# Kernel tuning notes

Measured on AMD Instinct MI355X. Metric: run time of the kernel, lower is better.

Reference implementation:

```python
import jax, jax.numpy as jnp
import numpy as np

B, P, D, H = 4, 2048, 768, 12  # batch, patches, patch_dims, heads
HD = D // H
EPS = 1e-5


def _layernorm(x, g, b):
    mu = jnp.mean(x, axis=-1, keepdims=True)
    var = jnp.mean(jnp.square(x - mu), axis=-1, keepdims=True)
    return (x - mu) * jax.lax.rsqrt(var + EPS) * g + b


def setup_inputs() -> dict:
    key = jax.random.key(0)
    ks = jax.random.split(key, 4)
    s = 0.02
    return {
        "x": jax.random.normal(ks[0], (B, P, D), jnp.float32),
        "ln1_w": jnp.ones((D,), jnp.float32),
        "ln1_b": jnp.zeros((D,), jnp.float32),
        "w_qkv": jax.random.normal(ks[1], (D, 3 * D), jnp.float32) * s,
        "b_qkv": jnp.zeros((3 * D,), jnp.float32),
        "ln2_w": jnp.ones((D,), jnp.float32),
        "ln2_b": jnp.zeros((D,), jnp.float32),
        "w_fc1": jax.random.normal(ks[2], (D, 4 * D), jnp.float32) * s,
        "b_fc1": jnp.zeros((4 * D,), jnp.float32),
        "w_fc2": jax.random.normal(ks[3], (4 * D, D), jnp.float32) * s,
        "b_fc2": jnp.zeros((D,), jnp.float32),
    }


def reference(x, ln1_w, ln1_b, w_qkv, b_qkv, ln2_w, ln2_b, w_fc1, b_fc1, w_fc2, b_fc2):
    scale = HD ** -0.5
    # --- attention block (pre-norm) ---
    residual = x
    h = _layernorm(x, ln1_w, ln1_b)
    qkv = h @ w_qkv + b_qkv                              # (B, P, 3D)
    qkv = qkv.reshape(B, P, 3, H, HD).transpose(2, 0, 3, 1, 4)  # (3, B, H, P, HD)
    q, k, v = qkv[0], qkv[1], qkv[2]
    attn = jnp.einsum('bhpd,bhqd->bhpq', q, k) * scale   # (B, H, P, P)
    # NOTE: original uses nn.Softmax(dim=1) -> normalizes over HEADS axis
    attn = jax.nn.softmax(attn, axis=1)
    out = jnp.einsum('bhpq,bhqd->bhpd', attn, v)         # (B, H, P, HD)
    out = out.transpose(0, 2, 1, 3).reshape(B, P, D)
    x = out + residual
    # --- MLP block (pre-norm) ---
    residual = x
    h = _layernorm(x, ln2_w, ln2_b)
    h = jax.nn.gelu(h @ w_fc1 + b_fc1, approximate=False)
    h = h @ w_fc2 + b_fc2
    return h + residual
```

## Files before the change

### kernel.cpp

```cpp
#include <hip/hip_runtime.h>
#include <hip/hip_bf16.h>

typedef __bf16 bf8 __attribute__((ext_vector_type(8)));
typedef float f4 __attribute__((ext_vector_type(4)));
typedef unsigned short u16;
typedef unsigned int u32;

#define B_ 4
#define P_ 2048
#define D_ 768
#define H_ 12
#define HD_ 64
#define EXPC_ 0.18033688011112042f

typedef const __attribute__((address_space(1))) void gvoid;
typedef __attribute__((address_space(3))) void lvoid;

__device__ __forceinline__ void gl_lds16(const u16* g, u16* l) {
  __builtin_amdgcn_global_load_lds((gvoid*)g, (lvoid*)l, 16, 0, 0);
}

__device__ __forceinline__ u16 f2bf(float f) {
  union { float f; u32 u; } c; c.f = f;
  u32 u = c.u;
  u += 0x7fffu + ((u >> 16) & 1u);
  return (u16)(u >> 16);
}

__device__ __forceinline__ float bf2f(u16 v) {
  union { u32 u; float f; } c; c.u = (u32)v << 16; return c.f;
}

__device__ __forceinline__ uint2 pack4(f4 v) {
  union { float f; u32 u; } a, b, c, d;
  a.f = v[0]; b.f = v[1]; c.f = v[2]; d.f = v[3];
  uint2 r;
  r.x = (a.u >> 16) | (b.u & 0xffff0000u);
  r.y = (c.u >> 16) | (d.u & 0xffff0000u);
  return r;
}

__device__ __forceinline__ f4 unpack4(ushort4 v) {
  f4 r;
  r[0] = bf2f(v.x); r[1] = bf2f(v.y); r[2] = bf2f(v.z); r[3] = bf2f(v.w);
  return r;
}

__device__ __forceinline__ f4 unp2(uint2 u) {
  f4 r;
  r[0] = bf2f((u16)(u.x & 0xffffu)); r[1] = bf2f((u16)(u.x >> 16));
  r[2] = bf2f((u16)(u.y & 0xffffu)); r[3] = bf2f((u16)(u.y >> 16));
  return r;
}

__device__ __forceinline__ bf8 mkbf8(f4 a, f4 b) {
  union { uint4 u; bf8 v; } c;
  uint2 l = pack4(a), h = pack4(b);
  c.u = make_uint4(l.x, l.y, h.x, h.y);
  return c.v;
}

__device__ __forceinline__ f4 mfma16(bf8 a, bf8 b, f4 c) {
  return __builtin_amdgcn_mfma_f32_16x16x32_bf16(a, b, c, 0, 0, 0);
}

#define ZERO44(acc)                    \
  {                                    \
    f4 z_ = {0.f, 0.f, 0.f, 0.f};      \
    for (int i_ = 0; i_ < 4; ++i_)     \
      for (int j_ = 0; j_ < 4; ++j_)   \
        acc[i_][j_] = z_;              \
  }

__device__ __forceinline__ int xcd_swz(int lin, int nwg) {
  return (lin & 7) * (nwg >> 3) + (lin >> 3);
}

__global__ __launch_bounds__(256) void prep_k(const float* __restrict__ wqkv, u16* __restrict__ wqkvT,
                                              const float* __restrict__ wfc1, u16* __restrict__ wfc1T,
                                              const float* __restrict__ wfc2, u16* __restrict__ wfc2T,
                                              const float* __restrict__ x, const float* __restrict__ g,
                                              const float* __restrict__ b, u16* __restrict__ hln) {
  __shared__ float t[32][33];
  __shared__ float a[4], a2[4];
  int id = blockIdx.x;
  if (id >= 6336) {
    int row = id - 6336;
    const float* xr = x + (size_t)row * D_;
    float v0 = xr[threadIdx.x], v1 = xr[threadIdx.x + 256], v2 = xr[threadIdx.x + 512];
    float s = v0 + v1 + v2;
    float s2 = v0 * v0 + v1 * v1 + v2 * v2;
    #pragma unroll
    for (int o = 32; o > 0; o >>= 1) {
      s += __shfl_down(s, o, 64);
      s2 += __shfl_down(s2, o, 64);
    }
    int wv = threadIdx.x >> 6;
    if ((threadIdx.x & 63) == 0) { a[wv] = s; a2[wv] = s2; }
    __syncthreads();
    s = a[0] + a[1] + a[2] + a[3];
    s2 = a2[0] + a2[1] + a2[2] + a2[3];
    float mean = s * (1.f / 768.f);
    float var = s2 * (1.f / 768.f) - mean * mean;
    float rstd = rsqrtf(var + 1e-5f);
    u16* orow = hln + (size_t)row * D_;
    float vv[3] = {v0, v1, v2};
    #pragma unroll
    for (int j = 0; j < 3; ++j) {
      int i = threadIdx.x + j * 256;
      orow[i] = f2bf((vv[j] - mean) * rstd * g[i] + b[i]);
    }
    return;
  }
  const float* src;
  u16* dst;
  int R, C, bx, by;
  if (id < 1728) {
    src = wqkv; dst = wqkvT; R = 768; C = 2304; bx = id % 72; by = id / 72;
  } else if (id < 4032) {
    int j = id - 1728;
    src = wfc1; dst = wfc1T; R = 768; C = 3072; bx = j % 96; by = j / 96;
  } else {
    int j = id - 4032;
    src = wfc2; dst = wfc2T; R = 3072; C = 768; bx = j % 24; by = j / 24;
  }
  int c0 = bx * 32, r0 = by * 32;
  int tx = threadIdx.x & 31, ty = threadIdx.x >> 5;
  #pragma unroll
  for (int i = 0; i < 32; i += 8) {
    int r = r0 + ty + i, c = c0 + tx;
    t[ty + i][tx] = (r < R && c < C) ? src[(size_t)r * C + c] : 0.f;
  }
  __syncthreads();
  #pragma unroll
  for (int i = 0; i < 32; i += 8) {
    int c = c0 + ty + i, r = r0 + tx;
    if (c < C && r < R) dst[(size_t)c * R + r] = f2bf(t[tx][ty + i]);
  }
}

__global__ __launch_bounds__(256) void ln2add_k(const float* __restrict__ x,
                                                const u16* __restrict__ O0,
                                                const u16* __restrict__ O1,
                                                const float* __restrict__ g,
                                                const float* __restrict__ b,
                                                float* __restrict__ x2,
                                                u16* __restrict__ out) {
  int row = blockIdx.x;
  const float* xr = x + (size_t)row * D_;
  const u16* o0 = O0 + (size_t)row * D_;
  const u16* o1 = O1 + (size_t)row * D_;
  float vv[3];
  #pragma unroll
  for (int j = 0; j < 3; ++j) {
    int i = threadIdx.x + j * 256;
    vv[j] = xr[i] + bf2f(o0[i]) + bf2f(o1[i]);
  }
  float s = vv[0] + vv[1] + vv[2];
  float s2 = vv[0] * vv[0] + vv[1] * vv[1] + vv[2] * vv[2];
  #pragma unroll
  for (int o = 32; o > 0; o >>= 1) {
    s += __shfl_down(s, o, 64);
    s2 += __shfl_down(s2, o, 64);
  }
  __shared__ float a[4], a2[4];
  int wv = threadIdx.x >> 6;
  if ((threadIdx.x & 63) == 0) { a[wv] = s; a2[wv] = s2; }
  __syncthreads();
  s = a[0] + a[1] + a[2] + a[3];
  s2 = a2[0] + a2[1] + a2[2] + a2[3];
  float mean = s * (1.f / 768.f);
  float var = s2 * (1.f / 768.f) - mean * mean;
  float rstd = rsqrtf(var + 1e-5f);
  float* x2r = x2 + (size_t)row * D_;
  u16* orow = out + (size_t)row * D_;
  #pragma unroll
  for (int j = 0; j < 3; ++j) {
    int i = threadIdx.x + j * 256;
    x2r[i] = vv[j];
    orow[i] = f2bf((vv[j] - mean) * rstd * g[i] + b[i]);
  }
}

template <int K>
__device__ __forceinline__ void staged_core(const u16* __restrict__ Ab,
                                            const u16* __restrict__ Bb,
                                            u16* As, u16* Bs, f4 acc[4][4]) {
  const int wave = threadIdx.x >> 6, lane = threadIdx.x & 63;
  const int l15 = lane & 15, quad = lane >> 4;
  const int lrow = lane >> 2;
  const int lcol = (lane & 3) * 8;
  const int mw = (wave & 1) * 64, nw = (wave >> 1) * 64;
#define STAGE_(k0_, buf_)                                                       \
  {                                                                             \
    u16* Ad_ = As + (buf_) * 128 * 32;                                          \
    u16* Bd_ = Bs + (buf_) * 128 * 32;                                          \
    const u16* ga_ = Ab + (size_t)(wave * 32 + lrow) * K + (k0_) + lcol;        \
    gl_lds16(ga_, &Ad_[(wave * 32) * 32]);                                      \
    gl_lds16(ga_ + (size_t)16 * K, &Ad_[(wave * 32 + 16) * 32]);                \
    const u16* gb_ = Bb + (size_t)(wave * 32 + lrow) * K + (k0_) + lcol;        \
    gl_lds16(gb_, &Bd_[(wave * 32) * 32]);                                      \
    gl_lds16(gb_ + (size_t)16 * K, &Bd_[(wave * 32 + 16) * 32]);                \
  }
  STAGE_(0, 0);
  __syncthreads();
  int cur = 0;
  for (int k0 = 0; k0 < K; k0 += 32) {
    if (k0 + 32 < K) STAGE_(k0 + 32, cur ^ 1);
    const u16* Ac = As + cur * 128 * 32;
    const u16* Bc = Bs + cur * 128 * 32;
    bf8 a[4], b[4];
    #pragma unroll
    for (int mt = 0; mt < 4; ++mt)
      a[mt] = *reinterpret_cast<const bf8*>(&Ac[(mw + mt * 16 + l15) * 32 + quad * 8]);
    #pragma unroll
    for (int nt = 0; nt < 4; ++nt)
      b[nt] = *reinterpret_cast<const bf8*>(&Bc[(nw + nt * 16 + l15) * 32 + quad * 8]);
    __builtin_amdgcn_s_setprio(1);
    #pragma unroll
    for (int mt = 0; mt < 4; ++mt)
      #pragma unroll
      for (int nt = 0; nt < 4; ++nt)
        acc[mt][nt] = mfma16(a[mt], b[nt], acc[mt][nt]);
    __builtin_amdgcn_s_setprio(0);
    __syncthreads();
    cur ^= 1;
  }
#undef STAGE_
}

__global__ __launch_bounds__(256) void gemm_qkv_k(const u16* __restrict__ hln,
                                                  const u16* __restrict__ wT,
                                                  const float* __restrict__ bias,
                                                  u16* __restrict__ Q, u16* __restrict__ Km,
                                                  u16* __restrict__ Vt) {
  __shared__ u16 As[2 * 128 * 32], Bs[2 * 128 * 32];
  int lin = blockIdx.y * gridDim.x + blockIdx.x;
  int swz = xcd_swz(lin, gridDim.x * gridDim.y);
  int m0 = (swz / gridDim.x) * 128, n0 = (swz % gridDim.x) * 128;
  f4 acc[4][4];
  ZERO44(acc);
  staged_core<768>(hln + (size_t)m0 * 768, wT + (size_t)n0 * 768, As, Bs, acc);
  int wave = threadIdx.x >> 6, lane = threadIdx.x & 63, l15 = lane & 15, quad = lane >> 4;
  int mW = m0 + (wave & 1) * 64, nW = n0 + (wave >> 1) * 64;
  #pragma unroll
  for (int mt = 0; mt < 4; ++mt)
    #pragma unroll
    for (int nt = 0; nt < 4; ++nt)
      #pragma unroll
      for (int r = 0; r < 4; ++r) {
        int m = mW + mt * 16 + quad * 4 + r;
        int n = nW + nt * 16 + l15;
        float v = acc[mt][nt][r] + bias[n];
        u16 bv = f2bf(v);
        int b = m >> 11, p = m & 2047;
        int which = n / 768, hn = n % 768;
        int h = hn >> 6, d = hn & 63;
        if (which == 0)
          Q[((size_t)(b * H_ + h) * P_ + p) * HD_ + d] = bv;
        else if (which == 1)
          Km[((size_t)(b * H_ + h) * P_ + p) * HD_ + d] = bv;
        else
          Vt[((size_t)(b * H_ + h) * HD_ + d) * P_ + p] = bv;
      }
}

__global__ __launch_bounds__(256) void gemm_fc1_k(const u16* __restrict__ A,
                                                  const u16* __restrict__ wT,
                                                  const float* __restrict__ bias,
                                                  u16* __restrict__ out) {
  __shared__ u16 As[2 * 128 * 32], Bs[2 * 128 * 32];
  int lin = blockIdx.y * gridDim.x + blockIdx.x;
  int swz = xcd_swz(lin, gridDim.x * gridDim.y);
  int m0 = (swz / gridDim.x) * 128, n0 = (swz % gridDim.x) * 128;
  f4 acc[4][4];
  ZERO44(acc);
  staged_core<768>(A + (size_t)m0 * 768, wT + (size_t)n0 * 768, As, Bs, acc);
  int wave = threadIdx.x >> 6, lane = threadIdx.x & 63, l15 = lane & 15, quad = lane >> 4;
  int mW = m0 + (wave & 1) * 64, nW = n0 + (wave >> 1) * 64;
  #pragma unroll
  for (int mt = 0; mt < 4; ++mt)
    #pragma unroll
    for (int nt = 0; nt < 4; ++nt)
      #pragma unroll
      for (int r = 0; r < 4; ++r) {
        int m = mW + mt * 16 + quad * 4 + r;
        int n = nW + nt * 16 + l15;
        float v = acc[mt][nt][r] + bias[n];
        float vv = v * v;
        float e = v * fmaf(0.1029434f, vv, 2.3022082f);
        float tt = __builtin_amdgcn_exp2f(e);
        float th = fmaf(-2.f, __builtin_amdgcn_rcpf(tt + 1.f), 1.f);
        v = 0.5f * v * (1.f + th);
        out[(size_t)m * 3072 + n] = f2bf(v);
      }
}

__global__ __launch_bounds__(256) void gemm_fc2_k(const u16* __restrict__ A,
                                                  const u16* __restrict__ wT,
                                                  const float* __restrict__ bias,
                                                  const float* __restrict__ resid,
                                                  float* __restrict__ out) {
  __shared__ u16 As[2 * 128 * 32], Bs[2 * 64 * 32];
  int wave = threadIdx.x >> 6, lane = threadIdx.x & 63, l15 = lane & 15, quad = lane >> 4;
  int lrow = lane >> 2, lcol = (lane & 3) * 8;
  int lin = blockIdx.y * gridDim.x + blockIdx.x;
  int swz = xcd_swz(lin, gridDim.x * gridDim.y);
  int m0 = (swz / gridDim.x) * 128, n0 = (swz % gridDim.x) * 64;
  const u16* Ab = A + (size_t)m0 * 3072;
  const u16* Bb = wT + (size_t)n0 * 3072;
  int mw = (wave & 1) * 64, nw = (wave >> 1) * 32;
  f4 acc[4][2];
  #pragma unroll
  for (int i = 0; i < 4; ++i)
    #pragma unroll
    for (int j = 0; j < 2; ++j) acc[i][j] = f4{0.f, 0.f, 0.f, 0.f};
#define STAGE2_(k0_, buf_)                                                      \
  {                                                                             \
    u16* Ad_ = As + (buf_) * 128 * 32;                                          \
    u16* Bd_ = Bs + (buf_) * 64 * 32;                                           \
    const u16* ga_ = Ab + (size_t)(wave * 32 + lrow) * 3072 + (k0_) + lcol;     \
    gl_lds16(ga_, &Ad_[(wave * 32) * 32]);                                      \
    gl_lds16(ga_ + (size_t)16 * 3072, &Ad_[(wave * 32 + 16) * 32]);             \
    const u16* gb_ = Bb + (size_t)(wave * 16 + lrow) * 3072 + (k0_) + lcol;     \
    gl_lds16(gb_, &Bd_[(wave * 16) * 32]);                                      \
  }
  STAGE2_(0, 0);
  __syncthreads();
  int cur = 0;
  for (int k0 = 0; k0 < 3072; k0 += 32) {
    if (k0 + 32 < 3072) STAGE2_(k0 + 32, cur ^ 1);
    const u16* Ac = As + cur * 128 * 32;
    const u16* Bc = Bs + cur * 64 * 32;
    bf8 a[4], b[2];
    #pragma unroll
    for (int mt = 0; mt < 4; ++mt)
      a[mt] = *reinterpret_cast<const bf8*>(&Ac[(mw + mt * 16 + l15) * 32 + quad * 8]);
    #pragma unroll
    for (int nt = 0; nt < 2; ++nt)
      b[nt] = *reinterpret_cast<const bf8*>(&Bc[(nw + nt * 16 + l15) * 32 + quad * 8]);
    __builtin_amdgcn_s_setprio(1);
    #pragma unroll
    for (int mt = 0; mt < 4; ++mt)
      #pragma unroll
      for (int nt = 0; nt < 2; ++nt)
        acc[mt][nt] = mfma16(a[mt], b[nt], acc[mt][nt]);
    __builtin_amdgcn_s_setprio(0);
    __syncthreads();
    cur ^= 1;
  }
#undef STAGE2_
  int mW = m0 + mw, nW = n0 + nw;
  #pragma unroll
  for (int mt = 0; mt < 4; ++mt)
    #pragma unroll
    for (int nt = 0; nt < 2; ++nt)
      #pragma unroll
      for (int r = 0; r < 4; ++r) {
        int m = mW + mt * 16 + quad * 4 + r;
        int n = nW + nt * 16 + l15;
        size_t idx = (size_t)m * 768 + n;
        out[idx] = acc[mt][nt][r] + bias[n] + resid[idx];
      }
}

__global__ __launch_bounds__(768) void attn_fused_k(const u16* __restrict__ Q,
                                                    const u16* __restrict__ Km,
                                                    const u16* __restrict__ Vt,
                                                    u16* __restrict__ O0,
                                                    u16* __restrict__ O1) {
  int id = blockIdx.x;
  int g = id & 7, pt = id >> 3;
  int b = g >> 1, qs = g & 1;
  int w = threadIdx.x >> 6, lane = threadIdx.x & 63, l15 = lane & 15, quad = lane >> 4;
  __shared__ __align__(16) u16 E[12][64][36];
  __shared__ __align__(16) float R[64][36];

  const u16* Qp = Q + ((size_t)(b * H_ + w) * P_ + pt * 64) * HD_;
  const u16* Kbase = Km + ((size_t)(b * H_ + w) * P_ + qs * 1024) * HD_;
  const u16* Vbase = Vt + (size_t)(b * H_ + w) * HD_ * P_ + qs * 1024;

  bf8 qf[4][2];
  #pragma unroll
  for (int nt = 0; nt < 4; ++nt)
    #pragma unroll
    for (int ks = 0; ks < 2; ++ks)
      qf[nt][ks] = *reinterpret_cast<const bf8*>(Qp + (size_t)(nt * 16 + l15) * HD_ + ks * 32 + quad * 8);

  f4 oacc[4][4];
  ZERO44(oacc);

  for (int qt = 0; qt < 32; ++qt) {
    const u16* Kp = Kbase + (size_t)qt * 32 * HD_;
    bf8 kf[2][2];
    #pragma unroll
    for (int mt = 0; mt < 2; ++mt)
      #pragma unroll
      for (int ks = 0; ks < 2; ++ks)
        kf[mt][ks] = *reinterpret_cast<const bf8*>(Kp + (size_t)(mt * 16 + l15) * HD_ + ks * 32 + quad * 8);
    bf8 vf[4];
    #pragma unroll
    for (int dt = 0; dt < 4; ++dt)
      vf[dt] = *reinterpret_cast<const bf8*>(Vbase + (size_t)(dt * 16 + l15) * P_ + qt * 32 + quad * 8);
    #pragma unroll
    for (int mt = 0; mt < 2; ++mt) {
      f4 s[4];
      #pragma unroll
      for (int nt = 0; nt < 4; ++nt) s[nt] = f4{0.f, 0.f, 0.f, 0.f};
      __builtin_amdgcn_s_setprio(1);
      #pragma unroll
      for (int nt = 0; nt < 4; ++nt) {
        s[nt] = mfma16(kf[mt][0], qf[nt][0], s[nt]);
        s[nt] = mfma16(kf[mt][1], qf[nt][1], s[nt]);
      }
      __builtin_amdgcn_s_setprio(0);
      #pragma unroll
      for (int nt = 0; nt < 4; ++nt) {
        f4 e;
        #pragma unroll
        for (int r = 0; r < 4; ++r) e[r] = __builtin_amdgcn_exp2f(s[nt][r] * EXPC_);
        *reinterpret_cast<uint2*>(&E[w][nt * 16 + l15][mt * 16 + quad * 4]) = pack4(e);
      }
    }
    __syncthreads();
    if (threadIdx.x < 512) {
      int p = threadIdx.x >> 3, qc = (threadIdx.x & 7) * 4;
      f4 sum = {0.f, 0.f, 0.f, 0.f};
      #pragma unroll
      for (int h = 0; h < 12; ++h)
        sum += unpack4(*reinterpret_cast<const ushort4*>(&E[h][p][qc]));
      f4 rc;
      #pragma unroll
      for (int c = 0; c < 4; ++c) rc[c] = __builtin_amdgcn_rcpf(sum[c]);
      *reinterpret_cast<f4*>(&R[p][qc]) = rc;
    }
    __syncthreads();
    #pragma unroll
    for (int pi = 0; pi < 4; ++pi) {
      int pp = pi * 16 + l15;
      uint2 e0 = *reinterpret_cast<const uint2*>(&E[w][pp][quad * 8]);
      uint2 e1 = *reinterpret_cast<const uint2*>(&E[w][pp][quad * 8 + 4]);
      f4 r0 = *reinterpret_cast<const f4*>(&R[pp][quad * 8]);
      f4 r1 = *reinterpret_cast<const f4*>(&R[pp][quad * 8 + 4]);
      bf8 af = mkbf8(unp2(e0) * r0, unp2(e1) * r1);
      __builtin_amdgcn_s_setprio(1);
      #pragma unroll
      for (int dt = 0; dt < 4; ++dt)
        oacc[dt][pi] = mfma16(vf[dt], af, oacc[dt][pi]);
      __builtin_amdgcn_s_setprio(0);
    }
  }
  __syncthreads();
  u16(*Os)[64][72] = reinterpret_cast<u16(*)[64][72]>(&E[0][0][0]);
  u16* Op = qs ? O1 : O0;
  #pragma unroll
  for (int hh = 0; hh < 2; ++hh) {
    if (w >= hh * 6 && w < hh * 6 + 6) {
      int wp = w - hh * 6;
      #pragma unroll
      for (int dt = 0; dt < 4; ++dt)
        #pragma unroll
        for (int pi = 0; pi < 4; ++pi)
          *reinterpret_cast<uint2*>(&Os[wp][pi * 16 + l15][dt * 16 + quad * 4]) = pack4(oacc[dt][pi]);
    }
    __syncthreads();
    #pragma unroll
    for (int j = 0; j < 4; ++j) {
      int c = threadIdx.x + j * 768;
      int p = c / 48, m = c % 48;
      int hp = m >> 3, d = (m & 7) * 8;
      uint4 val = *reinterpret_cast<const uint4*>(&Os[hp][p][d]);
      size_t go = (((size_t)b * P_) + pt * 64 + p) * D_ + (hh * 6 + hp) * 64 + d;
      *reinterpret_cast<uint4*>(Op + go) = val;
    }
    __syncthreads();
  }
}

extern "C" void kernel_launch(void* const* d_in, const int* in_sizes, int n_in,
                              void* d_out, int out_size, void* d_ws, size_t ws_size,
                              hipStream_t stream) {
  const float* x = (const float*)d_in[0];
  const float* ln1w = (const float*)d_in[1];
  const float* ln1b = (const float*)d_in[2];
  const float* wqkv = (const float*)d_in[3];
  const float* bqkv = (const float*)d_in[4];
  const float* ln2w = (const float*)d_in[5];
  const float* ln2b = (const float*)d_in[6];
  const float* wfc1 = (const float*)d_in[7];
  const float* bfc1 = (const float*)d_in[8];
  const float* wfc2 = (const float*)d_in[9];
  const float* bfc2 = (const float*)d_in[10];
  float* out = (float*)d_out;

  char* ws = (char*)d_ws;
  size_t off = 0;
  auto alloc = [&](size_t bytes) -> void* {
    void* p = ws + off;
    off += (bytes + 255) & ~(size_t)255;
    return p;
  };
  u16* hln = (u16*)alloc((size_t)8192 * 768 * 2);
  u16* wqkvT = (u16*)alloc((size_t)2304 * 768 * 2);
  u16* wfc1T = (u16*)alloc((size_t)3072 * 768 * 2);
  u16* wfc2T = (u16*)alloc((size_t)768 * 3072 * 2);
  u16* Qb = (u16*)alloc((size_t)B_ * H_ * P_ * HD_ * 2);
  u16* Kb = (u16*)alloc((size_t)B_ * H_ * P_ * HD_ * 2);
  u16* Vtb = (u16*)alloc((size_t)B_ * H_ * HD_ * P_ * 2);
  float* x2 = (float*)alloc((size_t)8192 * 768 * 4);
  u16* O0 = (u16*)alloc((size_t)8192 * 768 * 2);
  u16* O1 = (u16*)alloc((size_t)8192 * 768 * 2);
  u16* gbuf = (u16*)alloc((size_t)8192 * 3072 * 2);

  prep_k<<<14528, 256, 0, stream>>>(wqkv, wqkvT, wfc1, wfc1T, wfc2, wfc2T,
                                    x, ln1w, ln1b, hln);
  gemm_qkv_k<<<dim3(18, 64), 256, 0, stream>>>(hln, wqkvT, bqkv, Qb, Kb, Vtb);
  attn_fused_k<<<256, 768, 0, stream>>>(Qb, Kb, Vtb, O0, O1);
  ln2add_k<<<8192, 256, 0, stream>>>(x, O0, O1, ln2w, ln2b, x2, hln);
  gemm_fc1_k<<<dim3(24, 64), 256, 0, stream>>>(hln, wfc1T, bfc1, gbuf);
  gemm_fc2_k<<<dim3(12, 64), 256, 0, stream>>>(gbuf, wfc2T, bfc2, x2, out);
}
```

Measured before the change: 444.1 us.

## Triple-buffer GEMM LDS staging with single barrier per step; vectorize LN2

The GEMM mainloops move from double-buffered staging with two syncs per k-step to a three-stage ring buffer. Prefetch runs two tiles ahead, and an explicit s_waitcnt vmcnt plus one s_barrier replaces __syncthreads, so global-to-LDS loads overlap more with MFMA work. The ln2add kernel now uses 192 threads doing float4/ushort4 vector loads and stores instead of three scalar strided accesses per thread. The cost is 50% more LDS per GEMM block, which may lower occupancy, and hand-counted vmcnt values that must match the number of outstanding loads.

Measured after the change: 453.1 us. +2.0%, slower.

```diff
diff --git a/kernel.cpp b/kernel.cpp
--- a/kernel.cpp
+++ b/kernel.cpp
@@ -139,7 +139,7 @@
   }
 }
 
-__global__ __launch_bounds__(256) void ln2add_k(const float* __restrict__ x,
+__global__ __launch_bounds__(192) void ln2add_k(const float* __restrict__ x,
                                                 const u16* __restrict__ O0,
                                                 const u16* __restrict__ O1,
                                                 const float* __restrict__ g,
@@ -147,39 +147,40 @@
                                                 float* __restrict__ x2,
                                                 u16* __restrict__ out) {
   int row = blockIdx.x;
-  const float* xr = x + (size_t)row * D_;
-  const u16* o0 = O0 + (size_t)row * D_;
-  const u16* o1 = O1 + (size_t)row * D_;
-  float vv[3];
-  #pragma unroll
-  for (int j = 0; j < 3; ++j) {
-    int i = threadIdx.x + j * 256;
-    vv[j] = xr[i] + bf2f(o0[i]) + bf2f(o1[i]);
-  }
-  float s = vv[0] + vv[1] + vv[2];
-  float s2 = vv[0] * vv[0] + vv[1] * vv[1] + vv[2] * vv[2];
+  int i4 = threadIdx.x * 4;
+  const float4 xv = *reinterpret_cast<const float4*>(x + (size_t)row * D_ + i4);
+  ushort4 a0 = *reinterpret_cast<const ushort4*>(O0 + (size_t)row * D_ + i4);
+  ushort4 a1 = *reinterpret_cast<const ushort4*>(O1 + (size_t)row * D_ + i4);
+  f4 v;
+  v[0] = xv.x + bf2f(a0.x) + bf2f(a1.x);
+  v[1] = xv.y + bf2f(a0.y) + bf2f(a1.y);
+  v[2] = xv.z + bf2f(a0.z) + bf2f(a1.z);
+  v[3] = xv.w + bf2f(a0.w) + bf2f(a1.w);
+  float s = v[0] + v[1] + v[2] + v[3];
+  float s2 = v[0] * v[0] + v[1] * v[1] + v[2] * v[2] + v[3] * v[3];
   #pragma unroll
   for (int o = 32; o > 0; o >>= 1) {
     s += __shfl_down(s, o, 64);
     s2 += __shfl_down(s2, o, 64);
   }
-  __shared__ float a[4], a2[4];
+  __shared__ float a[3], a2[3];
   int wv = threadIdx.x >> 6;
   if ((threadIdx.x & 63) == 0) { a[wv] = s; a2[wv] = s2; }
   __syncthreads();
-  s = a[0] + a[1] + a[2] + a[3];
-  s2 = a2[0] + a2[1] + a2[2] + a2[3];
+  s = a[0] + a[1] + a[2];
+  s2 = a2[0] + a2[1] + a2[2];
   float mean = s * (1.f / 768.f);
   float var = s2 * (1.f / 768.f) - mean * mean;
   float rstd = rsqrtf(var + 1e-5f);
-  float* x2r = x2 + (size_t)row * D_;
-  u16* orow = out + (size_t)row * D_;
-  #pragma unroll
-  for (int j = 0; j < 3; ++j) {
-    int i = threadIdx.x + j * 256;
-    x2r[i] = vv[j];
-    orow[i] = f2bf((vv[j] - mean) * rstd * g[i] + b[i]);
-  }
+  *reinterpret_cast<float4*>(x2 + (size_t)row * D_ + i4) = make_float4(v[0], v[1], v[2], v[3]);
+  f4 nv;
+  const float4 gv = *reinterpret_cast<const float4*>(g + i4);
+  const float4 bv = *reinterpret_cast<const float4*>(b + i4);
+  nv[0] = (v[0] - mean) * rstd * gv.x + bv.x;
+  nv[1] = (v[1] - mean) * rstd * gv.y + bv.y;
+  nv[2] = (v[2] - mean) * rstd * gv.z + bv.z;
+  nv[3] = (v[3] - mean) * rstd * gv.w + bv.w;
+  *reinterpret_cast<uint2*>(out + (size_t)row * D_ + i4) = pack4(nv);
 }
 
 template <int K>
@@ -191,42 +192,49 @@
   const int lrow = lane >> 2;
   const int lcol = (lane & 3) * 8;
   const int mw = (wave & 1) * 64, nw = (wave >> 1) * 64;
-#define STAGE_(k0_, buf_)                                                       \
+  constexpr int NK = K / 32;
+#define STAGE_(t)                                                               \
   {                                                                             \
-    u16* Ad_ = As + (buf_) * 128 * 32;                                          \
-    u16* Bd_ = Bs + (buf_) * 128 * 32;                                          \
-    const u16* ga_ = Ab + (size_t)(wave * 32 + lrow) * K + (k0_) + lcol;        \
+    int buf_ = (t) % 3;                                                         \
+    u16* Ad_ = As + buf_ * 128 * 32;                                            \
+    u16* Bd_ = Bs + buf_ * 128 * 32;                                            \
+    const u16* ga_ = Ab + (size_t)(wave * 32 + lrow) * K + (t) * 32 + lcol;     \
     gl_lds16(ga_, &Ad_[(wave * 32) * 32]);                                      \
     gl_lds16(ga_ + (size_t)16 * K, &Ad_[(wave * 32 + 16) * 32]);                \
-    const u16* gb_ = Bb + (size_t)(wave * 32 + lrow) * K + (k0_) + lcol;        \
+    const u16* gb_ = Bb + (size_t)(wave * 32 + lrow) * K + (t) * 32 + lcol;     \
     gl_lds16(gb_, &Bd_[(wave * 32) * 32]);                                      \
     gl_lds16(gb_ + (size_t)16 * K, &Bd_[(wave * 32 + 16) * 32]);                \
   }
-  STAGE_(0, 0);
-  __syncthreads();
-  int cur = 0;
-  for (int k0 = 0; k0 < K; k0 += 32) {
-    if (k0 + 32 < K) STAGE_(k0 + 32, cur ^ 1);
-    const u16* Ac = As + cur * 128 * 32;
-    const u16* Bc = Bs + cur * 128 * 32;
-    bf8 a[4], b[4];
-    #pragma unroll
-    for (int mt = 0; mt < 4; ++mt)
-      a[mt] = *reinterpret_cast<const bf8*>(&Ac[(mw + mt * 16 + l15) * 32 + quad * 8]);
-    #pragma unroll
-    for (int nt = 0; nt < 4; ++nt)
-      b[nt] = *reinterpret_cast<const bf8*>(&Bc[(nw + nt * 16 + l15) * 32 + quad * 8]);
-    __builtin_amdgcn_s_setprio(1);
-    #pragma unroll
-    for (int mt = 0; mt < 4; ++mt)
-      #pragma unroll
-      for (int nt = 0; nt < 4; ++nt)
-        acc[mt][nt] = mfma16(a[mt], b[nt], acc[mt][nt]);
-    __builtin_amdgcn_s_setprio(0);
-    __syncthreads();
-    cur ^= 1;
-  }
+#define COMP_(t)                                                                \
+  {                                                                             \
+    const u16* Ac_ = As + ((t) % 3) * 128 * 32;                                 \
+    const u16* Bc_ = Bs + ((t) % 3) * 128 * 32;                                 \
+    bf8 a_[4], b_[4];                                                           \
+    _Pragma("unroll")                                                           \
+    for (int mt_ = 0; mt_ < 4; ++mt_)                                           \
+      a_[mt_] = *reinterpret_cast<const bf8*>(&Ac_[(mw + mt_ * 16 + l15) * 32 + quad * 8]); \
+    _Pragma("unroll")                                                           \
+    for (int nt_ = 0; nt_ < 4; ++nt_)                                           \
+      b_[nt_] = *reinterpret_cast<const bf8*>(&Bc_[(nw + nt_ * 16 + l15) * 32 + quad * 8]); \
+    __builtin_amdgcn_s_setprio(1);                                              \
+    _Pragma("unroll")                                                           \
+    for (int mt_ = 0; mt_ < 4; ++mt_)                                           \
+      _Pragma("unroll")                                                         \
+      for (int nt_ = 0; nt_ < 4; ++nt_)                                         \
+        acc[mt_][nt_] = mfma16(a_[mt_], b_[nt_], acc[mt_][nt_]);                \
+    __builtin_amdgcn_s_setprio(0);                                              \
+  }
+  STAGE_(0);
+  STAGE_(1);
+  for (int k = 0; k < NK - 1; ++k) {
+    asm volatile("s_waitcnt vmcnt(4)\n\ts_barrier" ::: "memory");
+    if (k + 2 < NK) STAGE_(k + 2);
+    COMP_(k);
+  }
+  asm volatile("s_waitcnt vmcnt(0)\n\ts_barrier" ::: "memory");
+  COMP_(NK - 1);
 #undef STAGE_
+#undef COMP_
 }
 
 __global__ __launch_bounds__(256) void gemm_qkv_k(const u16* __restrict__ hln,
@@ -234,7 +242,7 @@
                                                   const float* __restrict__ bias,
                                                   u16* __restrict__ Q, u16* __restrict__ Km,
                                                   u16* __restrict__ Vt) {
-  __shared__ u16 As[2 * 128 * 32], Bs[2 * 128 * 32];
+  __shared__ u16 As[3 * 128 * 32], Bs[3 * 128 * 32];
   int lin = blockIdx.y * gridDim.x + blockIdx.x;
   int swz = xcd_swz(lin, gridDim.x * gridDim.y);
   int m0 = (swz / gridDim.x) * 128, n0 = (swz % gridDim.x) * 128;
@@ -269,7 +277,7 @@
                                                   const u16* __restrict__ wT,
                                                   const float* __restrict__ bias,
                                                   u16* __restrict__ out) {
-  __shared__ u16 As[2 * 128 * 32], Bs[2 * 128 * 32];
+  __shared__ u16 As[3 * 128 * 32], Bs[3 * 128 * 32];
   int lin = blockIdx.y * gridDim.x + blockIdx.x;
   int swz = xcd_swz(lin, gridDim.x * gridDim.y);
   int m0 = (swz / gridDim.x) * 128, n0 = (swz % gridDim.x) * 128;
@@ -301,7 +309,7 @@
                                                   const float* __restrict__ bias,
                                                   const float* __restrict__ resid,
                                                   float* __restrict__ out) {
-  __shared__ u16 As[2 * 128 * 32], Bs[2 * 64 * 32];
+  __shared__ u16 As[3 * 128 * 32], Bs[3 * 64 * 32];
   int wave = threadIdx.x >> 6, lane = threadIdx.x & 63, l15 = lane & 15, quad = lane >> 4;
   int lrow = lane >> 2, lcol = (lane & 3) * 8;
   int lin = blockIdx.y * gridDim.x + blockIdx.x;
@@ -315,41 +323,47 @@
   for (int i = 0; i < 4; ++i)
     #pragma unroll
     for (int j = 0; j < 2; ++j) acc[i][j] = f4{0.f, 0.f, 0.f, 0.f};
-#define STAGE2_(k0_, buf_)                                                      \
+#define STAGE2_(t)                                                              \
   {                                                                             \
-    u16* Ad_ = As + (buf_) * 128 * 32;                                          \
-    u16* Bd_ = Bs + (buf_) * 64 * 32;                                           \
-    const u16* ga_ = Ab + (size_t)(wave * 32 + lrow) * 3072 + (k0_) + lcol;     \
+    int buf_ = (t) % 3;                                                         \
+    u16* Ad_ = As + buf_ * 128 * 32;                                            \
+    u16* Bd_ = Bs + buf_ * 64 * 32;                                             \
+    const u16* ga_ = Ab + (size_t)(wave * 32 + lrow) * 3072 + (t) * 32 + lcol;  \
     gl_lds16(ga_, &Ad_[(wave * 32) * 32]);                                      \
     gl_lds16(ga_ + (size_t)16 * 3072, &Ad_[(wave * 32 + 16) * 32]);             \
-    const u16* gb_ = Bb + (size_t)(wave * 16 + lrow) * 3072 + (k0_) + lcol;     \
+    const u16* gb_ = Bb + (size_t)(wave * 16 + lrow) * 3072 + (t) * 32 + lcol;  \
     gl_lds16(gb_, &Bd_[(wave * 16) * 32]);                                      \
   }
-  STAGE2_(0, 0);
-  __syncthreads();
-  int cur = 0;
-  for (int k0 = 0; k0 < 3072; k0 += 32) {
-    if (k0 + 32 < 3072) STAGE2_(k0 + 32, cur ^ 1);
-    const u16* Ac = As + cur * 128 * 32;
-    const u16* Bc = Bs + cur * 64 * 32;
-    bf8 a[4], b[2];
-    #pragma unroll
-    for (int mt = 0; mt < 4; ++mt)
-      a[mt] = *reinterpret_cast<const bf8*>(&Ac[(mw + mt * 16 + l15) * 32 + quad * 8]);
-    #pragma unroll
-    for (int nt = 0; nt < 2; ++nt)
-      b[nt] = *reinterpret_cast<const bf8*>(&Bc[(nw + nt * 16 + l15) * 32 + quad * 8]);
-    __builtin_amdgcn_s_setprio(1);
-    #pragma unroll
-    for (int mt = 0; mt < 4; ++mt)
-      #pragma unroll
-      for (int nt = 0; nt < 2; ++nt)
-        acc[mt][nt] = mfma16(a[mt], b[nt], acc[mt][nt]);
-    __builtin_amdgcn_s_setprio(0);
-    __syncthreads();
-    cur ^= 1;
-  }
+#define COMP2_(t)                                                               \
+  {                                                                             \
+    const u16* Ac_ = As + ((t) % 3) * 128 * 32;                                 \
+    const u16* Bc_ = Bs + ((t) % 3) * 64 * 32;                                  \
+    bf8 a_[4], b_[2];                                                           \
+    _Pragma("unroll")                                                           \
+    for (int mt_ = 0; mt_ < 4; ++mt_)                                           \
+      a_[mt_] = *reinterpret_cast<const bf8*>(&Ac_[(mw + mt_ * 16 + l15) * 32 + quad * 8]); \
+    _Pragma("unroll")                                                           \
+    for (int nt_ = 0; nt_ < 2; ++nt_)                                           \
+      b_[nt_] = *reinterpret_cast<const bf8*>(&Bc_[(nw + nt_ * 16 + l15) * 32 + quad * 8]); \
+    __builtin_amdgcn_s_setprio(1);                                              \
+    _Pragma("unroll")                                                           \
+    for (int mt_ = 0; mt_ < 4; ++mt_)                                           \
+      _Pragma("unroll")                                                         \
+      for (int nt_ = 0; nt_ < 2; ++nt_)                                         \
+        acc[mt_][nt_] = mfma16(a_[mt_], b_[nt_], acc[mt_][nt_]);                \
+    __builtin_amdgcn_s_setprio(0);                                              \
+  }
+  STAGE2_(0);
+  STAGE2_(1);
+  for (int k = 0; k < 95; ++k) {
+    asm volatile("s_waitcnt vmcnt(3)\n\ts_barrier" ::: "memory");
+    if (k + 2 < 96) STAGE2_(k + 2);
+    COMP2_(k);
+  }
+  asm volatile("s_waitcnt vmcnt(0)\n\ts_barrier" ::: "memory");
+  COMP2_(95);
 #undef STAGE2_
+#undef COMP2_
   int mW = m0 + mw, nW = n0 + nw;
   #pragma unroll
   for (int mt = 0; mt < 4; ++mt)
@@ -516,7 +530,7 @@
                                     x, ln1w, ln1b, hln);
   gemm_qkv_k<<<dim3(18, 64), 256, 0, stream>>>(hln, wqkvT, bqkv, Qb, Kb, Vtb);
   attn_fused_k<<<256, 768, 0, stream>>>(Qb, Kb, Vtb, O0, O1);
-  ln2add_k<<<8192, 256, 0, stream>>>(x, O0, O1, ln2w, ln2b, x2, hln);
+  ln2add_k<<<8192, 192, 0, stream>>>(x, O0, O1, ln2w, ln2b, x2, hln);
   gemm_fc1_k<<<dim3(24, 64), 256, 0, stream>>>(hln, wfc1T, bfc1, gbuf);
   gemm_fc2_k<<<dim3(12, 64), 256, 0, stream>>>(gbuf, wfc2T, bfc2, x2, out);
 }
```
